# Kernel tuning notes

Hardware: AMD Instinct MI355X
Metric: run time of the kernel (lower is better)

Reference implementation:

```python
import jax, jax.numpy as jnp
import numpy as np

N, C, D = 131072, 1024, 64

def setup_inputs() -> dict:
    key = jax.random.key(0)
    k1, k2, k3 = jax.random.split(key, 3)
    inputs = jax.random.normal(k1, (N, D), dtype=jnp.float32)
    centers = jax.random.normal(k2, (C, D), dtype=jnp.float32)
    coefs = jax.random.uniform(k3, (C,), dtype=jnp.float32) / C
    max_avg_distance = jnp.ones((1,), dtype=jnp.float32)
    return {"inputs": inputs, "centers": centers, "coefs": coefs,
            "max_avg_distance": max_avg_distance}

def _pairwise_l2(x, c):
    x2 = jnp.sum(x * x, axis=-1, keepdims=True)          # (N, 1)
    c2 = jnp.sum(c * c, axis=-1)                          # (C,)
    d2 = x2 + c2 - 2.0 * jnp.einsum('nd,cd->nc', x, c)    # (N, C)
    return jnp.sqrt(jnp.maximum(d2, 0.0))

def reference(inputs, centers, coefs, max_avg_distance):
    x = inputs.reshape(inputs.shape[0], -1)               # flatten(inputs, 1)
    distances = _pairwise_l2(x, centers)                  # (N, C)
    c = jnp.abs(coefs)
    s = jnp.sum(c)
    c = jnp.where(s == 0.0, c, c / s)                     # normalize unless sum==0
    weighted_avg = distances @ c                          # (N,)
    return max_avg_distance - weighted_avg                # broadcast (1,)-(N,) -> (N,)
```

## Files before the change

### kernel.cpp

```cpp
#include <hip/hip_runtime.h>
#include <hip/hip_bf16.h>
#include <cstdint>

#define DIM 64
#define NC  1024

typedef __attribute__((ext_vector_type(8))) __bf16 bf16x8;
typedef __attribute__((ext_vector_type(8))) short short8;
typedef __attribute__((ext_vector_type(4))) float f32x4;

static __device__ __forceinline__ unsigned short f32_to_bf16_rne(float f) {
    unsigned int u = __builtin_bit_cast(unsigned int, f);
    unsigned int r = u + 0x7FFFu + ((u >> 16) & 1u);
    return (unsigned short)(r >> 16);
}

__global__ __launch_bounds__(64) void prep_kernel(
    const float* __restrict__ coefs,
    const float* __restrict__ centers,
    float2* __restrict__ wc2,
    short8* __restrict__ bfrag)
{
    const int tid = threadIdx.x;

    if (blockIdx.x == 0) {
        float a[16];
        float s = 0.0f;
#pragma unroll
        for (int q = 0; q < 4; ++q) {
            f32x4 v = *(const f32x4*)(coefs + tid * 16 + q * 4);
#pragma unroll
            for (int j = 0; j < 4; ++j) {
                a[q * 4 + j] = fabsf(v[j]);
                s += a[q * 4 + j];
            }
        }
        s += __shfl_xor(s, 1, 64);
        s += __shfl_xor(s, 2, 64);
        s += __shfl_xor(s, 4, 64);
        s += __shfl_xor(s, 8, 64);
        s += __shfl_xor(s, 16, 64);
        s += __shfl_xor(s, 32, 64);
        const float inv = (s == 0.0f) ? 1.0f : (1.0f / s);
#pragma unroll
        for (int j = 0; j < 16; ++j)
            wc2[tid * 16 + j].x = a[j] * inv;
        return;
    }

    const int c = (blockIdx.x - 1) * 64 + tid;
    const float4* row = (const float4*)(centers + (size_t)c * DIM);

    float vals[DIM];
    float c2 = 0.0f;
#pragma unroll
    for (int q = 0; q < DIM / 4; ++q) {
        float4 v = row[q];
        vals[q * 4 + 0] = v.x; vals[q * 4 + 1] = v.y;
        vals[q * 4 + 2] = v.z; vals[q * 4 + 3] = v.w;
        c2 = fmaf(v.x, v.x, c2); c2 = fmaf(v.y, v.y, c2);
        c2 = fmaf(v.z, v.z, c2); c2 = fmaf(v.w, v.w, c2);
    }
    wc2[c].y = c2;

    const int tile = c >> 4;
    const int colL = c & 15;
#pragma unroll
    for (int kb = 0; kb < 2; ++kb) {
#pragma unroll
        for (int h = 0; h < 4; ++h) {
            short8 p;
#pragma unroll
            for (int j = 0; j < 8; ++j) {
                float v = -2.0f * vals[kb * 32 + h * 8 + j];
                p[j] = (short)f32_to_bf16_rne(v);
            }
            bfrag[(tile * 2 + kb) * 64 + (h * 16 + colL)] = p;
        }
    }
}

__global__ __launch_bounds__(256, 4) void dist_kernel(
    const float* __restrict__ x,
    const float2* __restrict__ wc2,
    const bf16x8* __restrict__ bfrag,
    const float* __restrict__ madp,
    float* __restrict__ out)
{
    const int lane = threadIdx.x & 63;
    const int wave = threadIdx.x >> 6;
    const int lo = lane & 15;
    const int hi = lane >> 4;
    const int pairIdx = wave >> 1;
    const int halfC  = wave & 1;
    const int rowBase = blockIdx.x * 128 + pairIdx * 64;

    __shared__ float part[4][64];

    bf16x8 afrag[4][2];
    float x2v[4][4];

#pragma unroll
    for (int g = 0; g < 4; ++g) {
        const int row = rowBase + g * 16 + lo;
        const float* rp = x + (size_t)row * DIM + hi * 8;
        float s2 = 0.0f;
#pragma unroll
        for (int kb = 0; kb < 2; ++kb) {
            f32x4 v0 = __builtin_nontemporal_load((const f32x4*)(rp + kb * 32));
            f32x4 v1 = __builtin_nontemporal_load((const f32x4*)(rp + kb * 32 + 4));
            float vv[8] = {v0.x, v0.y, v0.z, v0.w, v1.x, v1.y, v1.z, v1.w};
            short8 p;
#pragma unroll
            for (int j = 0; j < 8; ++j) {
                s2 = fmaf(vv[j], vv[j], s2);
                p[j] = (short)f32_to_bf16_rne(vv[j]);
            }
            afrag[g][kb] = __builtin_bit_cast(bf16x8, p);
        }
        s2 += __shfl_xor(s2, 16, 64);
        s2 += __shfl_xor(s2, 32, 64);
#pragma unroll
        for (int b = 0; b < 4; ++b)
            x2v[g][b] = __shfl(s2, hi * 4 + b, 64);
    }

    float sum[4][4];
#pragma unroll
    for (int g = 0; g < 4; ++g)
#pragma unroll
        for (int b = 0; b < 4; ++b) sum[g][b] = 0.0f;

    const int tbase = halfC * 32;
    const bf16x8* bp = bfrag + lane;
    const float2* wp = wc2 + lo;

    bf16x8 pb0[2], pb1[2];
    float2 pwc[2];
#pragma unroll
    for (int s = 0; s < 2; ++s) {
        const int t = tbase + s;
        pb0[s] = bp[t * 128];
        pb1[s] = bp[t * 128 + 64];
        pwc[s] = wp[t * 16];
    }

#pragma unroll 1
    for (int i = 0; i < 32; i += 2) {
        const float2 wcA = pwc[0], wcB = pwc[1];
        const bf16x8 a00 = pb0[0], a01 = pb1[0];
        const bf16x8 a10 = pb0[1], a11 = pb1[1];

        {
            const int n0 = i + 2, n1 = i + 3;
            const int t0 = tbase + ((n0 < 32) ? n0 : 0);
            const int t1 = tbase + ((n1 < 32) ? n1 : 0);
            pb0[0] = bp[t0 * 128]; pb1[0] = bp[t0 * 128 + 64]; pwc[0] = wp[t0 * 16];
            pb0[1] = bp[t1 * 128]; pb1[1] = bp[t1 * 128 + 64]; pwc[1] = wp[t1 * 16];
        }

        f32x4 acc0[4], acc1[4];
#pragma unroll
        for (int g = 0; g < 4; ++g)
#pragma unroll
            for (int b = 0; b < 4; ++b) {
                acc0[g][b] = x2v[g][b] + wcA.y;
                acc1[g][b] = x2v[g][b] + wcB.y;
            }

#pragma unroll
        for (int g = 0; g < 4; ++g)
            acc0[g] = __builtin_amdgcn_mfma_f32_16x16x32_bf16(afrag[g][0], a00, acc0[g], 0, 0, 0);
#pragma unroll
        for (int g = 0; g < 4; ++g)
            acc1[g] = __builtin_amdgcn_mfma_f32_16x16x32_bf16(afrag[g][0], a10, acc1[g], 0, 0, 0);
#pragma unroll
        for (int g = 0; g < 4; ++g)
            acc0[g] = __builtin_amdgcn_mfma_f32_16x16x32_bf16(afrag[g][1], a01, acc0[g], 0, 0, 0);
#pragma unroll
        for (int g = 0; g < 4; ++g)
            acc1[g] = __builtin_amdgcn_mfma_f32_16x16x32_bf16(afrag[g][1], a11, acc1[g], 0, 0, 0);

#pragma unroll
        for (int g = 0; g < 4; ++g)
#pragma unroll
            for (int b = 0; b < 4; ++b) {
                float d = __builtin_amdgcn_sqrtf(fabsf(acc0[g][b]));
                sum[g][b] = fmaf(wcA.x, d, sum[g][b]);
            }
#pragma unroll
        for (int g = 0; g < 4; ++g)
#pragma unroll
            for (int b = 0; b < 4; ++b) {
                float d = __builtin_amdgcn_sqrtf(fabsf(acc1[g][b]));
                sum[g][b] = fmaf(wcB.x, d, sum[g][b]);
            }
    }

#pragma unroll
    for (int g = 0; g < 4; ++g) {
#pragma unroll
        for (int b = 0; b < 4; ++b) {
            float v = sum[g][b];
            v += __shfl_xor(v, 1, 64);
            v += __shfl_xor(v, 2, 64);
            v += __shfl_xor(v, 4, 64);
            v += __shfl_xor(v, 8, 64);
            if (lo == 0) part[wave][g * 16 + hi * 4 + b] = v;
        }
    }
    __syncthreads();

    const int tid = threadIdx.x;
    if (tid < 128) {
        const int p = tid >> 6;
        const int r = tid & 63;
        const float s = part[2 * p][r] + part[2 * p + 1][r];
        __builtin_nontemporal_store(madp[0] - s, &out[blockIdx.x * 128 + p * 64 + r]);
    }
}

extern "C" void kernel_launch(void* const* d_in, const int* in_sizes, int n_in,
                              void* d_out, int out_size, void* d_ws, size_t ws_size,
                              hipStream_t stream) {
    const float* x       = (const float*)d_in[0];
    const float* centers = (const float*)d_in[1];
    const float* coefs   = (const float*)d_in[2];
    const float* mad     = (const float*)d_in[3];
    float* out = (float*)d_out;

    float2* wc2   = (float2*)d_ws;
    short8* bfrag = (short8*)((char*)d_ws + NC * sizeof(float2));

    const int N = in_sizes[0] / DIM;

    prep_kernel<<<1 + NC / 64, 64, 0, stream>>>(coefs, centers, wc2, bfrag);
    dist_kernel<<<N / 128, 256, 0, stream>>>(x, wc2, (const bf16x8*)bfrag, mad, out);
}
```

Measured before the change: 43.14 us.

## Stage center fragments in LDS and give each wave all centers for its rows

Each wave now owns 64 rows and loops over all 1024 centers instead of splitting centers between a wave pair. The bf16 center fragments are staged into 64KB of shared memory in two halves, and the weights/norms go to LDS, replacing per-wave global/L2 loads. This removes the cross-wave partial-sum reduction and halves the grid. In exchange it adds block-wide barriers with serialized staging and no overlap, and ~72KB of LDS per block, which limits occupancy to a couple of blocks per CU.

```diff
diff --git a/kernel.cpp b/kernel.cpp
--- a/kernel.cpp
+++ b/kernel.cpp
@@ -83,23 +83,29 @@
 __global__ __launch_bounds__(256, 4) void dist_kernel(
     const float* __restrict__ x,
     const float2* __restrict__ wc2,
-    const bf16x8* __restrict__ bfrag,
+    const char* __restrict__ bfragB,
     const float* __restrict__ madp,
     float* __restrict__ out)
 {
-    const int lane = threadIdx.x & 63;
-    const int wave = threadIdx.x >> 6;
+    const int tid  = threadIdx.x;
+    const int lane = tid & 63;
+    const int wave = tid >> 6;
     const int lo = lane & 15;
     const int hi = lane >> 4;
-    const int pairIdx = wave >> 1;
-    const int halfC  = wave & 1;
-    const int rowBase = blockIdx.x * 128 + pairIdx * 64;
-
-    __shared__ float part[4][64];
+    const int rowBase = blockIdx.x * 256 + wave * 64;
+
+    __shared__ __align__(16) char lbuf[65536];
+    __shared__ float2 wcl[NC];
+
+    {
+        const f32x4* wsrc = (const f32x4*)wc2;
+        f32x4* wdst = (f32x4*)wcl;
+        wdst[tid * 2]     = wsrc[tid * 2];
+        wdst[tid * 2 + 1] = wsrc[tid * 2 + 1];
+    }
 
     bf16x8 afrag[4][2];
     float x2v[4][4];
-
 #pragma unroll
     for (int g = 0; g < 4; ++g) {
         const int row = rowBase + g * 16 + lo;
@@ -131,72 +137,69 @@
 #pragma unroll
         for (int b = 0; b < 4; ++b) sum[g][b] = 0.0f;
 
-    const int tbase = halfC * 32;
-    const bf16x8* bp = bfrag + lane;
-    const float2* wp = wc2 + lo;
-
-    bf16x8 pb0[2], pb1[2];
-    float2 pwc[2];
-#pragma unroll
-    for (int s = 0; s < 2; ++s) {
-        const int t = tbase + s;
-        pb0[s] = bp[t * 128];
-        pb1[s] = bp[t * 128 + 64];
-        pwc[s] = wp[t * 16];
-    }
+    const char* lpB = lbuf + lane * 16;
 
 #pragma unroll 1
-    for (int i = 0; i < 32; i += 2) {
-        const float2 wcA = pwc[0], wcB = pwc[1];
-        const bf16x8 a00 = pb0[0], a01 = pb1[0];
-        const bf16x8 a10 = pb0[1], a11 = pb1[1];
-
+    for (int p = 0; p < 2; ++p) {
+        __syncthreads();
         {
-            const int n0 = i + 2, n1 = i + 3;
-            const int t0 = tbase + ((n0 < 32) ? n0 : 0);
-            const int t1 = tbase + ((n1 < 32) ? n1 : 0);
-            pb0[0] = bp[t0 * 128]; pb1[0] = bp[t0 * 128 + 64]; pwc[0] = wp[t0 * 16];
-            pb0[1] = bp[t1 * 128]; pb1[1] = bp[t1 * 128 + 64]; pwc[1] = wp[t1 * 16];
-        }
-
-        f32x4 acc0[4], acc1[4];
-#pragma unroll
-        for (int g = 0; g < 4; ++g)
-#pragma unroll
-            for (int b = 0; b < 4; ++b) {
-                acc0[g][b] = x2v[g][b] + wcA.y;
-                acc1[g][b] = x2v[g][b] + wcB.y;
-            }
-
-#pragma unroll
-        for (int g = 0; g < 4; ++g)
-            acc0[g] = __builtin_amdgcn_mfma_f32_16x16x32_bf16(afrag[g][0], a00, acc0[g], 0, 0, 0);
-#pragma unroll
-        for (int g = 0; g < 4; ++g)
-            acc1[g] = __builtin_amdgcn_mfma_f32_16x16x32_bf16(afrag[g][0], a10, acc1[g], 0, 0, 0);
-#pragma unroll
-        for (int g = 0; g < 4; ++g)
-            acc0[g] = __builtin_amdgcn_mfma_f32_16x16x32_bf16(afrag[g][1], a01, acc0[g], 0, 0, 0);
-#pragma unroll
-        for (int g = 0; g < 4; ++g)
-            acc1[g] = __builtin_amdgcn_mfma_f32_16x16x32_bf16(afrag[g][1], a11, acc1[g], 0, 0, 0);
-
-#pragma unroll
-        for (int g = 0; g < 4; ++g)
-#pragma unroll
-            for (int b = 0; b < 4; ++b) {
-                float d = __builtin_amdgcn_sqrtf(fabsf(acc0[g][b]));
-                sum[g][b] = fmaf(wcA.x, d, sum[g][b]);
-            }
-#pragma unroll
-        for (int g = 0; g < 4; ++g)
-#pragma unroll
-            for (int b = 0; b < 4; ++b) {
-                float d = __builtin_amdgcn_sqrtf(fabsf(acc1[g][b]));
-                sum[g][b] = fmaf(wcB.x, d, sum[g][b]);
-            }
-    }
-
+            const char* src = bfragB + (size_t)p * 65536 + tid * 16;
+            char* dst = lbuf + tid * 16;
+#pragma unroll
+            for (int k = 0; k < 16; ++k)
+                *(f32x4*)(dst + k * 4096) = *(const f32x4*)(src + k * 4096);
+        }
+        __syncthreads();
+
+#pragma unroll 1
+        for (int i = 0; i < 32; i += 2) {
+            const float2 wcA = wcl[p * 512 + i * 16 + lo];
+            const float2 wcB = wcl[p * 512 + (i + 1) * 16 + lo];
+            const bf16x8 a00 = *(const bf16x8*)(lpB + i * 2048);
+            const bf16x8 a01 = *(const bf16x8*)(lpB + i * 2048 + 1024);
+            const bf16x8 a10 = *(const bf16x8*)(lpB + i * 2048 + 2048);
+            const bf16x8 a11 = *(const bf16x8*)(lpB + i * 2048 + 3072);
+
+            f32x4 acc0[4], acc1[4];
+#pragma unroll
+            for (int g = 0; g < 4; ++g)
+#pragma unroll
+                for (int b = 0; b < 4; ++b) {
+                    acc0[g][b] = x2v[g][b] + wcA.y;
+                    acc1[g][b] = x2v[g][b] + wcB.y;
+                }
+
+#pragma unroll
+            for (int g = 0; g < 4; ++g)
+                acc0[g] = __builtin_amdgcn_mfma_f32_16x16x32_bf16(afrag[g][0], a00, acc0[g], 0, 0, 0);
+#pragma unroll
+            for (int g = 0; g < 4; ++g)
+                acc1[g] = __builtin_amdgcn_mfma_f32_16x16x32_bf16(afrag[g][0], a10, acc1[g], 0, 0, 0);
+#pragma unroll
+            for (int g = 0; g < 4; ++g)
+                acc0[g] = __builtin_amdgcn_mfma_f32_16x16x32_bf16(afrag[g][1], a01, acc0[g], 0, 0, 0);
+#pragma unroll
+            for (int g = 0; g < 4; ++g)
+                acc1[g] = __builtin_amdgcn_mfma_f32_16x16x32_bf16(afrag[g][1], a11, acc1[g], 0, 0, 0);
+
+#pragma unroll
+            for (int g = 0; g < 4; ++g)
+#pragma unroll
+                for (int b = 0; b < 4; ++b) {
+                    float d = __builtin_amdgcn_sqrtf(fabsf(acc0[g][b]));
+                    sum[g][b] = fmaf(wcA.x, d, sum[g][b]);
+                }
+#pragma unroll
+            for (int g = 0; g < 4; ++g)
+#pragma unroll
+                for (int b = 0; b < 4; ++b) {
+                    float d = __builtin_amdgcn_sqrtf(fabsf(acc1[g][b]));
+                    sum[g][b] = fmaf(wcB.x, d, sum[g][b]);
+                }
+        }
+    }
+
+    const float mad = madp[0];
 #pragma unroll
     for (int g = 0; g < 4; ++g) {
 #pragma unroll
@@ -206,17 +209,10 @@
             v += __shfl_xor(v, 2, 64);
             v += __shfl_xor(v, 4, 64);
             v += __shfl_xor(v, 8, 64);
-            if (lo == 0) part[wave][g * 16 + hi * 4 + b] = v;
-        }
-    }
-    __syncthreads();
-
-    const int tid = threadIdx.x;
-    if (tid < 128) {
-        const int p = tid >> 6;
-        const int r = tid & 63;
-        const float s = part[2 * p][r] + part[2 * p + 1][r];
-        __builtin_nontemporal_store(madp[0] - s, &out[blockIdx.x * 128 + p * 64 + r]);
+            if (lo == 0)
+                __builtin_nontemporal_store(mad - v,
+                    &out[rowBase + g * 16 + hi * 4 + b]);
+        }
     }
 }
 
@@ -235,5 +231,5 @@
     const int N = in_sizes[0] / DIM;
 
     prep_kernel<<<1 + NC / 64, 64, 0, stream>>>(coefs, centers, wc2, bfrag);
-    dist_kernel<<<N / 128, 256, 0, stream>>>(x, wc2, (const bf16x8*)bfrag, mad, out);
-}
+    dist_kernel<<<N / 256, 256, 0, stream>>>(x, wc2, (const char*)bfrag, mad, out);
+}
```

New measurement: 43.58 us. About the same (+1.0%).
